# Kernel optimization log

Hardware: AMD Instinct MI355X
Metric: run time of the kernel (lower is better)

The kernel has to match this reference:

```python
import jax, jax.numpy as jnp
import numpy as np

BIG = 1.0e8  # masked_fill value from the torch module


def setup_inputs() -> dict:
    key = jax.random.key(0)
    k1, k2, k3, k4 = jax.random.split(key, 4)
    B, N, M, D = 32, 2048, 2048, 3
    o_weights = jax.random.randint(k1, (B, N), 0, 2, dtype=jnp.int32)
    outputs = jax.random.normal(k2, (B, N, D), dtype=jnp.float32)
    t_weights = jax.random.randint(k3, (B, M), 0, 2, dtype=jnp.int32)
    targets = jax.random.normal(k4, (B, M, D), dtype=jnp.float32)
    return {"o_weights": o_weights, "outputs": outputs, "t_weights": t_weights, "targets": targets}


def _chamfer(mask_a, pc_a, mask_b, pc_b):
    # pairwise Euclidean distances [B, N, M] via ||a||^2 + ||b||^2 - 2 a.b
    a2 = jnp.sum(pc_a * pc_a, axis=-1)  # [B, N]
    b2 = jnp.sum(pc_b * pc_b, axis=-1)  # [B, M]
    ab = jnp.einsum("bnd,bmd->bnm", pc_a, pc_b)
    d2 = jnp.maximum(a2[..., :, None] + b2[..., None, :] - 2.0 * ab, 0.0)
    dist = jnp.sqrt(d2)  # [B, N, M]
    mm = (mask_a != 0)[..., :, None] & (mask_b != 0)[..., None, :]
    dist = jnp.where(mm, dist, BIG)
    ma = mask_a.astype(pc_a.dtype)
    mb = mask_b.astype(pc_b.dtype)
    min1 = jnp.min(dist, axis=-1) ** 2 * ma  # [B, N]
    min2 = jnp.min(dist, axis=-2) ** 2 * mb  # [B, M]
    return 0.5 * (jnp.sum(min1, axis=-1) + jnp.sum(min2, axis=-1))  # [B]


def reference(o_weights, outputs, t_weights, targets):
    return _chamfer(o_weights, outputs, t_weights, targets)
```

## Files before the change

kernel.cpp:

```cpp
#include <hip/hip_runtime.h>
#include <hip/hip_bf16.h>

#define B_   32
#define N_   2048
#define M_   2048
#define R_   16
#define GX_  32
#define BIG2 1.0e16f

__global__ __launch_bounds__(256) void chamfer_prep(
    const int* __restrict__ o_w, const float* __restrict__ o_pts,
    const int* __restrict__ t_w, const float* __restrict__ t_pts,
    float4* __restrict__ prep)
{
    int idx = blockIdx.x * 256 + threadIdx.x;
    int dir = idx / (B_ * M_);
    int r   = idx - dir * (B_ * M_);
    const int*   w = (dir == 0) ? t_w   : o_w;
    const float* p = (dir == 0) ? t_pts : o_pts;
    float x = p[r * 3 + 0];
    float y = p[r * 3 + 1];
    float z = p[r * 3 + 2];
    float n2 = fmaf(x, x, fmaf(y, y, z * z));
    float ww = (w[r] != 0) ? n2 : BIG2;
    prep[idx] = make_float4(-2.0f * x, -2.0f * y, -2.0f * z, ww);
}

__global__ __launch_bounds__(256) void chamfer_main(
    const int* __restrict__ o_w, const float* __restrict__ o_pts,
    const int* __restrict__ t_w, const float* __restrict__ t_pts,
    const float4* __restrict__ prep, float* __restrict__ partials)
{
    const int dir  = blockIdx.z;
    const int b    = blockIdx.y;
    const int lane = threadIdx.x & 63;
    const int wv   = threadIdx.x >> 6;
    const int row0 = (blockIdx.x * 4 + wv) * R_;

    const int*   __restrict__ wa = (dir == 0) ? o_w   : t_w;
    const float* __restrict__ pa = (dir == 0) ? o_pts : t_pts;
    const float4* __restrict__ pb = prep + (size_t)dir * (B_ * M_) + (size_t)b * M_;

    int base = __builtin_amdgcn_readfirstlane((b * N_ + row0) * 3);
    const float* rp = pa + base;
    float rx[R_], ry[R_], rz[R_];
    #pragma unroll
    for (int r = 0; r < R_; ++r) {
        rx[r] = rp[3 * r + 0];
        ry[r] = rp[3 * r + 1];
        rz[r] = rp[3 * r + 2];
    }

    float acc[R_];
    #pragma unroll
    for (int r = 0; r < R_; ++r) acc[r] = 3.4e38f;

    #pragma unroll 4
    for (int t = 0; t < M_ / 64; ++t) {
        float4 q = pb[t * 64 + lane];
        #pragma unroll
        for (int r = 0; r < R_; ++r) {
            float d = fmaf(rx[r], q.x, fmaf(ry[r], q.y, fmaf(rz[r], q.z, q.w)));
            acc[r] = fminf(acc[r], d);
        }
    }

    #pragma unroll
    for (int r = 0; r < R_; ++r) {
        float v = acc[r];
        #pragma unroll
        for (int off = 32; off; off >>= 1) v = fminf(v, __shfl_xor(v, off, 64));
        acc[r] = v;
    }

    int mbase = __builtin_amdgcn_readfirstlane(b * N_ + row0);
    const int* wp = wa + mbase;
    float sum = 0.0f;
    #pragma unroll
    for (int r = 0; r < R_; ++r) {
        float a2 = fmaf(rx[r], rx[r], fmaf(ry[r], ry[r], rz[r] * rz[r]));
        float d2 = fmaxf(a2 + acc[r], 0.0f);
        sum += (wp[r] != 0) ? d2 : 0.0f;
    }
    __shared__ float ws4[4];
    if (lane == 0) ws4[wv] = sum;
    __syncthreads();
    if (threadIdx.x == 0)
        partials[b * (2 * GX_) + dir * GX_ + blockIdx.x]
            = ws4[0] + ws4[1] + ws4[2] + ws4[3];
}

__global__ __launch_bounds__(256) void chamfer_finish(
    const float* __restrict__ partials, float* __restrict__ loss)
{
    int t = threadIdx.x;
    int b = t >> 3, k = t & 7;
    const float4* p4 = (const float4*)(partials + b * (2 * GX_) + k * 8);
    float4 u = p4[0], v = p4[1];
    float s = ((u.x + u.y) + (u.z + u.w)) + ((v.x + v.y) + (v.z + v.w));
    #pragma unroll
    for (int off = 4; off; off >>= 1) s += __shfl_xor(s, off, 64);
    if (k == 0) loss[b] = 0.5f * s;
}

__global__ void chamfer_zero(float* __restrict__ loss)
{
    if (threadIdx.x < B_) loss[threadIdx.x] = 0.0f;
}

__global__ __launch_bounds__(256) void chamfer_nolds(
    const int* __restrict__ o_w, const float* __restrict__ o_pts,
    const int* __restrict__ t_w, const float* __restrict__ t_pts,
    float* __restrict__ loss)
{
    const int dir  = blockIdx.z;
    const int b    = blockIdx.y;
    const int lane = threadIdx.x & 63;
    const int wv   = threadIdx.x >> 6;
    const int row0 = (blockIdx.x * 4 + wv) * R_;

    const int*   __restrict__ wa = (dir == 0) ? o_w   : t_w;
    const float* __restrict__ pa = (dir == 0) ? o_pts : t_pts;
    const int*   __restrict__ wb = (dir == 0) ? t_w   : o_w;
    const float* __restrict__ pb = (dir == 0) ? t_pts : o_pts;

    int base = __builtin_amdgcn_readfirstlane((b * N_ + row0) * 3);
    const float* rp = pa + base;
    float rx[R_], ry[R_], rz[R_];
    #pragma unroll
    for (int r = 0; r < R_; ++r) {
        rx[r] = rp[3 * r + 0];
        ry[r] = rp[3 * r + 1];
        rz[r] = rp[3 * r + 2];
    }
    float acc[R_];
    #pragma unroll
    for (int r = 0; r < R_; ++r) acc[r] = 3.4e38f;

    #pragma unroll 2
    for (int t = 0; t < M_ / 64; ++t) {
        int ib = b * M_ + t * 64 + lane;
        float bx = pb[ib * 3 + 0], by = pb[ib * 3 + 1], bz = pb[ib * 3 + 2];
        float n2 = fmaf(bx, bx, fmaf(by, by, bz * bz));
        float qw = (wb[ib] != 0) ? n2 : BIG2;
        float qx = -2.0f * bx, qy = -2.0f * by, qz = -2.0f * bz;
        #pragma unroll
        for (int r = 0; r < R_; ++r) {
            float d = fmaf(rx[r], qx, fmaf(ry[r], qy, fmaf(rz[r], qz, qw)));
            acc[r] = fminf(acc[r], d);
        }
    }
    #pragma unroll
    for (int r = 0; r < R_; ++r) {
        float v = acc[r];
        #pragma unroll
        for (int off = 32; off; off >>= 1) v = fminf(v, __shfl_xor(v, off, 64));
        acc[r] = v;
    }
    int mbase = __builtin_amdgcn_readfirstlane(b * N_ + row0);
    const int* wp = wa + mbase;
    float sum = 0.0f;
    #pragma unroll
    for (int r = 0; r < R_; ++r) {
        float a2 = fmaf(rx[r], rx[r], fmaf(ry[r], ry[r], rz[r] * rz[r]));
        float d2 = fmaxf(a2 + acc[r], 0.0f);
        sum += (wp[r] != 0) ? d2 : 0.0f;
    }
    if (lane == 0) atomicAdd(&loss[b], 0.5f * sum);
}

extern "C" void kernel_launch(void* const* d_in, const int* in_sizes, int n_in,
                              void* d_out, int out_size, void* d_ws, size_t ws_size,
                              hipStream_t stream) {
    const int*   o_w   = (const int*)  d_in[0];
    const float* o_pts = (const float*)d_in[1];
    const int*   t_w   = (const int*)  d_in[2];
    const float* t_pts = (const float*)d_in[3];
    float* loss = (float*)d_out;

    const size_t prep_bytes = (size_t)2 * B_ * M_ * sizeof(float4);
    const size_t part_bytes = (size_t)B_ * 2 * GX_ * sizeof(float);
    dim3 grid(GX_, B_, 2);

    if (ws_size >= prep_bytes + part_bytes) {
        float4* prep     = (float4*)d_ws;
        float*  partials = (float*)((char*)d_ws + prep_bytes);
        chamfer_prep<<<(2 * B_ * M_) / 256, 256, 0, stream>>>(
            o_w, o_pts, t_w, t_pts, prep);
        chamfer_main<<<grid, 256, 0, stream>>>(
            o_w, o_pts, t_w, t_pts, prep, partials);
        chamfer_finish<<<1, 256, 0, stream>>>(partials, loss);
    } else {
        chamfer_zero<<<1, 64, 0, stream>>>(loss);
        chamfer_nolds<<<grid, 256, 0, stream>>>(
            o_w, o_pts, t_w, t_pts, loss);
    }
}
```

Measured before the change: 92.01 us.

## Fuse prep into main kernel via LDS staging and packed float2 math

Removes the separate prep kernel and its global float4 workspace. Each 512-thread block now builds the transformed target points for its batch directly in shared memory (32 KB). Rows per wave drop from 16 to 8, and the inner distance/min loop uses 2-wide vector FMA/min, which can map to packed fp32 instructions. This saves one launch and a global round trip, at the cost of redundant per-block prep work (32 blocks per batch recompute the same LDS table) and a block-wide sync before compute.

```diff
diff --git a/kernel.cpp b/kernel.cpp
--- a/kernel.cpp
+++ b/kernel.cpp
@@ -1,93 +1,128 @@
 #include <hip/hip_runtime.h>
 #include <hip/hip_bf16.h>
 
-#define B_   32
-#define N_   2048
-#define M_   2048
-#define R_   16
-#define GX_  32
-#define BIG2 1.0e16f
-
-__global__ __launch_bounds__(256) void chamfer_prep(
+#define B_    32
+#define N_    2048
+#define M_    2048
+#define RW_   8
+#define GX_   32
+#define BIG2  1.0e16f
+
+typedef float v2f __attribute__((ext_vector_type(2)));
+
+__device__ __forceinline__ v2f v2_fma(v2f a, v2f b, v2f c) {
+#if __has_builtin(__builtin_elementwise_fma)
+    return __builtin_elementwise_fma(a, b, c);
+#else
+    v2f r; r.x = fmaf(a.x, b.x, c.x); r.y = fmaf(a.y, b.y, c.y); return r;
+#endif
+}
+__device__ __forceinline__ v2f v2_min(v2f a, v2f b) {
+#if __has_builtin(__builtin_elementwise_min)
+    return __builtin_elementwise_min(a, b);
+#else
+    v2f r; r.x = fminf(a.x, b.x); r.y = fminf(a.y, b.y); return r;
+#endif
+}
+
+__global__ __launch_bounds__(512, 8) void chamfer_main(
     const int* __restrict__ o_w, const float* __restrict__ o_pts,
     const int* __restrict__ t_w, const float* __restrict__ t_pts,
-    float4* __restrict__ prep)
-{
-    int idx = blockIdx.x * 256 + threadIdx.x;
-    int dir = idx / (B_ * M_);
-    int r   = idx - dir * (B_ * M_);
-    const int*   w = (dir == 0) ? t_w   : o_w;
-    const float* p = (dir == 0) ? t_pts : o_pts;
-    float x = p[r * 3 + 0];
-    float y = p[r * 3 + 1];
-    float z = p[r * 3 + 2];
-    float n2 = fmaf(x, x, fmaf(y, y, z * z));
-    float ww = (w[r] != 0) ? n2 : BIG2;
-    prep[idx] = make_float4(-2.0f * x, -2.0f * y, -2.0f * z, ww);
-}
-
-__global__ __launch_bounds__(256) void chamfer_main(
-    const int* __restrict__ o_w, const float* __restrict__ o_pts,
-    const int* __restrict__ t_w, const float* __restrict__ t_pts,
-    const float4* __restrict__ prep, float* __restrict__ partials)
+    float* __restrict__ partials)
 {
     const int dir  = blockIdx.z;
     const int b    = blockIdx.y;
-    const int lane = threadIdx.x & 63;
-    const int wv   = threadIdx.x >> 6;
-    const int row0 = (blockIdx.x * 4 + wv) * R_;
-
-    const int*   __restrict__ wa = (dir == 0) ? o_w   : t_w;
-    const float* __restrict__ pa = (dir == 0) ? o_pts : t_pts;
-    const float4* __restrict__ pb = prep + (size_t)dir * (B_ * M_) + (size_t)b * M_;
-
-    int base = __builtin_amdgcn_readfirstlane((b * N_ + row0) * 3);
-    const float* rp = pa + base;
-    float rx[R_], ry[R_], rz[R_];
-    #pragma unroll
-    for (int r = 0; r < R_; ++r) {
-        rx[r] = rp[3 * r + 0];
-        ry[r] = rp[3 * r + 1];
-        rz[r] = rp[3 * r + 2];
-    }
-
-    float acc[R_];
-    #pragma unroll
-    for (int r = 0; r < R_; ++r) acc[r] = 3.4e38f;
-
-    #pragma unroll 4
+    const int tid  = threadIdx.x;
+    const int lane = tid & 63;
+    const int wv   = tid >> 6;
+    const int row0 = blockIdx.x * (8 * RW_) + wv * RW_;
+
+    const int*   wa; const float* pa;
+    const int*   wb; const float* pb;
+    if (dir == 0) { wa = o_w; pa = o_pts; wb = t_w; pb = t_pts; }
+    else          { wa = t_w; pa = t_pts; wb = o_w; pb = o_pts; }
+
+    __shared__ float4 sq[M_];
+    __shared__ float  wsum[8];
+
+    {
+        const float2* src2 = (const float2*)(pb + (size_t)b * M_ * 3);
+        const int2*   wb2  = (const int2*)(wb + (size_t)b * M_);
+        #pragma unroll
+        for (int k = 0; k < 2; ++k) {
+            int p = tid + k * 512;
+            float2 u0 = src2[p * 3 + 0];
+            float2 u1 = src2[p * 3 + 1];
+            float2 u2 = src2[p * 3 + 2];
+            int2   mm = wb2[p];
+            float x0 = u0.x, y0 = u0.y, z0 = u1.x;
+            float x1 = u1.y, y1 = u2.x, z1 = u2.y;
+            float n20 = fmaf(x0, x0, fmaf(y0, y0, z0 * z0));
+            float n21 = fmaf(x1, x1, fmaf(y1, y1, z1 * z1));
+            sq[2 * p]     = make_float4(-2.f * x0, -2.f * y0, -2.f * z0,
+                                        mm.x ? n20 : BIG2);
+            sq[2 * p + 1] = make_float4(-2.f * x1, -2.f * y1, -2.f * z1,
+                                        mm.y ? n21 : BIG2);
+        }
+    }
+
+    v2f rx2[4], ry2[4], rz2[4];
+    {
+        const float* rp = pa + (size_t)(b * N_ + row0) * 3;
+        #pragma unroll
+        for (int j = 0; j < 4; ++j) {
+            rx2[j] = (v2f){ rp[(2 * j) * 3 + 0], rp[(2 * j + 1) * 3 + 0] };
+            ry2[j] = (v2f){ rp[(2 * j) * 3 + 1], rp[(2 * j + 1) * 3 + 1] };
+            rz2[j] = (v2f){ rp[(2 * j) * 3 + 2], rp[(2 * j + 1) * 3 + 2] };
+        }
+    }
+    __syncthreads();
+
+    v2f acc[4];
+    #pragma unroll
+    for (int j = 0; j < 4; ++j) acc[j] = (v2f){ 3.4e38f, 3.4e38f };
+
+    #pragma unroll 2
     for (int t = 0; t < M_ / 64; ++t) {
-        float4 q = pb[t * 64 + lane];
-        #pragma unroll
-        for (int r = 0; r < R_; ++r) {
-            float d = fmaf(rx[r], q.x, fmaf(ry[r], q.y, fmaf(rz[r], q.z, q.w)));
-            acc[r] = fminf(acc[r], d);
-        }
-    }
-
-    #pragma unroll
-    for (int r = 0; r < R_; ++r) {
-        float v = acc[r];
-        #pragma unroll
-        for (int off = 32; off; off >>= 1) v = fminf(v, __shfl_xor(v, off, 64));
-        acc[r] = v;
-    }
-
-    int mbase = __builtin_amdgcn_readfirstlane(b * N_ + row0);
-    const int* wp = wa + mbase;
+        float4 q = sq[t * 64 + lane];
+        v2f qx = (v2f){ q.x, q.x };
+        v2f qy = (v2f){ q.y, q.y };
+        v2f qz = (v2f){ q.z, q.z };
+        v2f qw = (v2f){ q.w, q.w };
+        #pragma unroll
+        for (int j = 0; j < 4; ++j) {
+            v2f d = v2_fma(rx2[j], qx, v2_fma(ry2[j], qy, v2_fma(rz2[j], qz, qw)));
+            acc[j] = v2_min(acc[j], d);
+        }
+    }
+
+    const int* wp = wa + (size_t)b * N_ + row0;
     float sum = 0.0f;
     #pragma unroll
-    for (int r = 0; r < R_; ++r) {
-        float a2 = fmaf(rx[r], rx[r], fmaf(ry[r], ry[r], rz[r] * rz[r]));
-        float d2 = fmaxf(a2 + acc[r], 0.0f);
-        sum += (wp[r] != 0) ? d2 : 0.0f;
-    }
-    __shared__ float ws4[4];
-    if (lane == 0) ws4[wv] = sum;
+    for (int j = 0; j < 4; ++j) {
+        float m0 = acc[j].x, m1 = acc[j].y;
+        #pragma unroll
+        for (int off = 32; off; off >>= 1) {
+            m0 = fminf(m0, __shfl_xor(m0, off, 64));
+            m1 = fminf(m1, __shfl_xor(m1, off, 64));
+        }
+        float a20 = fmaf(rx2[j].x, rx2[j].x,
+                    fmaf(ry2[j].x, ry2[j].x, rz2[j].x * rz2[j].x));
+        float a21 = fmaf(rx2[j].y, rx2[j].y,
+                    fmaf(ry2[j].y, ry2[j].y, rz2[j].y * rz2[j].y));
+        float d20 = fmaxf(a20 + m0, 0.0f);
+        float d21 = fmaxf(a21 + m1, 0.0f);
+        sum += (wp[2 * j]     != 0) ? d20 : 0.0f;
+        sum += (wp[2 * j + 1] != 0) ? d21 : 0.0f;
+    }
+    if (lane == 0) wsum[wv] = sum;
     __syncthreads();
-    if (threadIdx.x == 0)
-        partials[b * (2 * GX_) + dir * GX_ + blockIdx.x]
-            = ws4[0] + ws4[1] + ws4[2] + ws4[3];
+    if (tid == 0) {
+        float s = 0.f;
+        #pragma unroll
+        for (int i = 0; i < 8; ++i) s += wsum[i];
+        partials[((size_t)b * 2 + dir) * GX_ + blockIdx.x] = s;
+    }
 }
 
 __global__ __launch_bounds__(256) void chamfer_finish(
@@ -117,7 +152,7 @@
     const int b    = blockIdx.y;
     const int lane = threadIdx.x & 63;
     const int wv   = threadIdx.x >> 6;
-    const int row0 = (blockIdx.x * 4 + wv) * R_;
+    const int row0 = (blockIdx.x * 4 + wv) * 16;
 
     const int*   __restrict__ wa = (dir == 0) ? o_w   : t_w;
     const float* __restrict__ pa = (dir == 0) ? o_pts : t_pts;
@@ -126,16 +161,16 @@
 
     int base = __builtin_amdgcn_readfirstlane((b * N_ + row0) * 3);
     const float* rp = pa + base;
-    float rx[R_], ry[R_], rz[R_];
-    #pragma unroll
-    for (int r = 0; r < R_; ++r) {
+    float rx[16], ry[16], rz[16];
+    #pragma unroll
+    for (int r = 0; r < 16; ++r) {
         rx[r] = rp[3 * r + 0];
         ry[r] = rp[3 * r + 1];
         rz[r] = rp[3 * r + 2];
     }
-    float acc[R_];
-    #pragma unroll
-    for (int r = 0; r < R_; ++r) acc[r] = 3.4e38f;
+    float acc[16];
+    #pragma unroll
+    for (int r = 0; r < 16; ++r) acc[r] = 3.4e38f;
 
     #pragma unroll 2
     for (int t = 0; t < M_ / 64; ++t) {
@@ -145,13 +180,13 @@
         float qw = (wb[ib] != 0) ? n2 : BIG2;
         float qx = -2.0f * bx, qy = -2.0f * by, qz = -2.0f * bz;
         #pragma unroll
-        for (int r = 0; r < R_; ++r) {
+        for (int r = 0; r < 16; ++r) {
             float d = fmaf(rx[r], qx, fmaf(ry[r], qy, fmaf(rz[r], qz, qw)));
             acc[r] = fminf(acc[r], d);
         }
     }
     #pragma unroll
-    for (int r = 0; r < R_; ++r) {
+    for (int r = 0; r < 16; ++r) {
         float v = acc[r];
         #pragma unroll
         for (int off = 32; off; off >>= 1) v = fminf(v, __shfl_xor(v, off, 64));
@@ -161,7 +196,7 @@
     const int* wp = wa + mbase;
     float sum = 0.0f;
     #pragma unroll
-    for (int r = 0; r < R_; ++r) {
+    for (int r = 0; r < 16; ++r) {
         float a2 = fmaf(rx[r], rx[r], fmaf(ry[r], ry[r], rz[r] * rz[r]));
         float d2 = fmaxf(a2 + acc[r], 0.0f);
         sum += (wp[r] != 0) ? d2 : 0.0f;
@@ -178,20 +213,17 @@
     const float* t_pts = (const float*)d_in[3];
     float* loss = (float*)d_out;
 
-    const size_t prep_bytes = (size_t)2 * B_ * M_ * sizeof(float4);
     const size_t part_bytes = (size_t)B_ * 2 * GX_ * sizeof(float);
-    dim3 grid(GX_, B_, 2);
-
-    if (ws_size >= prep_bytes + part_bytes) {
-        float4* prep     = (float4*)d_ws;
-        float*  partials = (float*)((char*)d_ws + prep_bytes);
-        chamfer_prep<<<(2 * B_ * M_) / 256, 256, 0, stream>>>(
-            o_w, o_pts, t_w, t_pts, prep);
-        chamfer_main<<<grid, 256, 0, stream>>>(
-            o_w, o_pts, t_w, t_pts, prep, partials);
+
+    if (ws_size >= part_bytes) {
+        float* partials = (float*)d_ws;
+        dim3 grid(GX_, B_, 2);
+        chamfer_main<<<grid, 512, 0, stream>>>(
+            o_w, o_pts, t_w, t_pts, partials);
         chamfer_finish<<<1, 256, 0, stream>>>(partials, loss);
     } else {
         chamfer_zero<<<1, 64, 0, stream>>>(loss);
+        dim3 grid(N_ / 64, B_, 2);
         chamfer_nolds<<<grid, 256, 0, stream>>>(
             o_w, o_pts, t_w, t_pts, loss);
     }
```

New measurement: 90.81 us. Within noise of the previous version (-1.3%).
